# Optimization experiments

Hardware: AMD Instinct MI355X
Metric: run time of the kernel (lower is better)

## Reference

```python
import jax, jax.numpy as jnp
import numpy as np
from jax import lax

MINUS_INF = -1.0e9
BOS, EOS, PAD = 0, 1, 2
NB_LABELS, MAX_DEPTH, EXTRA = 96, 8, 3
STATE = NB_LABELS * MAX_DEPTH + EXTRA  # 771
B, T = 32, 128


def _init_transitions(key):
    t = jax.random.uniform(key, (STATE, STATE), minval=-0.1, maxval=0.1, dtype=jnp.float32)
    # structural constraints from init_weights()
    t = t.at[:, BOS].set(MINUS_INF)          # nothing transitions into BOS
    t = t.at[EOS, :].set(MINUS_INF)          # nothing leaves EOS
    t = t.at[BOS, NB_LABELS + EXTRA:].set(MINUS_INF)  # BOS only into depth-0 states
    t = t.at[NB_LABELS + EXTRA:, EOS].set(MINUS_INF)  # only depth-0 states into EOS
    t = t.at[PAD, :].set(MINUS_INF)
    t = t.at[NB_LABELS + EXTRA:, PAD].set(MINUS_INF)
    t = t.at[PAD, EOS].set(0.0)
    t = t.at[PAD, PAD].set(0.0)
    return t


def setup_inputs() -> dict:
    key = jax.random.key(0)
    k1, k2, k3 = jax.random.split(key, 3)
    emissions = jax.random.normal(k1, (B, T, STATE), dtype=jnp.float32)
    # valid (non-special) states only, so gold-path scores stay finite
    tags = jax.random.randint(k2, (B, T), EXTRA, STATE, dtype=jnp.int64)
    mask = jnp.ones((B, T), dtype=jnp.float32)
    transitions = _init_transitions(k3)
    return {"emissions": emissions, "tags": tags, "mask": mask, "transitions": transitions}


def _crf_nll(emissions, tags, mask, transitions):
    b, t, s = emissions.shape
    tags = tags.astype(jnp.int32)
    batch_idx = jnp.arange(b)

    # ---- gold path score ----
    first = tags[:, 0]
    scores = transitions[BOS, first] + emissions[batch_idx, 0, first]
    prev, cur = tags[:, :-1], tags[:, 1:]
    e_sc = jnp.take_along_axis(emissions[:, 1:], cur[..., None], axis=2)[..., 0]  # (B,T-1)
    t_sc = transitions[prev, cur]                                                 # (B,T-1)
    scores = scores + jnp.sum((e_sc + t_sc) * mask[:, 1:], axis=1)
    last_idx = mask.sum(axis=1).astype(jnp.int32) - 1
    last_tags = tags[batch_idx, last_idx]
    scores = scores + transitions[last_tags, EOS]

    # ---- log partition: forward algorithm (logsumexp DP over S x S) ----
    alphas0 = transitions[BOS][None, :] + emissions[:, 0]  # (B,S)

    def step(alphas, inp):
        em, m = inp  # em: (B,S), m: (B,)
        # (B,S_prev,1) + (S_prev,S_cur) + (B,1,S_cur) -> logsumexp over S_prev
        new = jax.scipy.special.logsumexp(
            alphas[:, :, None] + transitions[None, :, :] + em[:, None, :], axis=1)
        alphas = jnp.where(m[:, None] > 0, new, alphas)
        return alphas, None

    alphas, _ = lax.scan(step, alphas0,
                         (jnp.swapaxes(emissions[:, 1:], 0, 1), mask[:, 1:].T))
    log_z = jax.scipy.special.logsumexp(alphas + transitions[:, EOS][None, :], axis=1)

    # nll = -sum(score - logZ)
    return -jnp.sum(scores - log_z)


def reference(emissions, tags, mask, transitions):
    return _crf_nll(emissions, tags, mask, transitions)
```

## Files before the change

kernel.cpp:

```cpp
#include <hip/hip_runtime.h>
#include <math.h>

typedef unsigned long long u64;
typedef unsigned int u32;

static constexpr int S    = 771;
static constexpr int Tn   = 128;
static constexpr int Bn   = 32;
static constexpr int BOSs = 0;
static constexpr int EOSs = 1;

static constexpr int JB    = 7;
static constexpr int ROWS  = 128;
static constexpr int JPAD  = JB * ROWS;
static constexpr int NW    = 4;
static constexpr int KQ    = JPAD / NW;
static constexpr int KW    = KQ / 4;
static constexpr int KK    = KQ / 16;
static constexpr int NDATA = JPAD / 4;
static constexpr int NMAX  = JB * NW;
static constexpr int XSTR  = 256;
static constexpr int EBLK  = NW * KK * 2 * 64 * 16;
static constexpr int ETOT  = JB * EBLK;
static constexpr float CB  = 8.0f;
static constexpr float C0V = 4.5f;

__device__ __forceinline__ float wave_max_bfly(float v) {
    #pragma unroll
    for (int off = 32; off > 0; off >>= 1) v = fmaxf(v, __shfl_xor(v, off));
    return v;
}
__device__ __forceinline__ float wave_sum_f(float v) {
    #pragma unroll
    for (int off = 32; off > 0; off >>= 1) v += __shfl_down(v, off);
    return v;
}

__device__ __forceinline__ u64 ald64(const u64* p) {
    return __hip_atomic_load((u64*)p, __ATOMIC_RELAXED, __HIP_MEMORY_SCOPE_AGENT);
}
__device__ __forceinline__ void ast64(u64* p, u64 v) {
    __hip_atomic_store(p, v, __ATOMIC_RELAXED, __HIP_MEMORY_SCOPE_AGENT);
}
__device__ __forceinline__ u64 pack(unsigned tag, unsigned payload) {
    return ((u64)tag << 32) | (u64)payload;
}

#if __has_builtin(__builtin_amdgcn_sdot4)
__device__ __forceinline__ int dot4i(unsigned a, unsigned b, int c) {
    return __builtin_amdgcn_sdot4((int)a, (int)b, c, false);
}
#else
__device__ __forceinline__ int dot4i(unsigned a, unsigned b, int c) {
    c += (int)(a & 0xff)         * (int)(b & 0xff);
    c += (int)((a >> 8) & 0xff)  * (int)((b >> 8) & 0xff);
    c += (int)((a >> 16) & 0xff) * (int)((b >> 16) & 0xff);
    c += (int)((a >> 24) & 0xff) * (int)((b >> 24) & 0xff);
    return c;
}
#endif

extern "C" __global__ void build_tabs(const float* __restrict__ trans,
                                      unsigned char* __restrict__ eswz,
                                      float* __restrict__ eteos) {
    int idx = blockIdx.x * blockDim.x + threadIdx.x;
    if (idx < JPAD)
        eteos[idx] = (idx < S) ? __expf(trans[idx * S + EOSs]) : 0.f;
    if (idx >= ETOT) return;
    int e = idx & 15;
    int u = idx >> 4;
    int lane = u & 63;  u >>= 6;
    int rr = u & 1;     u >>= 1;
    int kk = u % KK;
    int h  = u / KK;
    int w  = h & 3, jb = h >> 2;
    int i = w * KQ + kk * 16 + e;
    int j = jb * ROWS + rr * 64 + lane;
    float v = 0.f;
    if (i < S && j < S) v = 115.f * __expf(trans[i * S + j]);
    int q8 = (int)(v + 0.5f);
    if (q8 > 127) q8 = 127;
    eswz[idx] = (unsigned char)q8;
}

__device__ __forceinline__ void publishW(u64* Wp, int jb, int w, unsigned tag,
                                         float af, float C, int lane) {
    float xf = fminf(127.f, 127.f * __expf(af - C));
    int xi = (int)(xf + 0.5f);
    int b0 = __shfl(xi, (4 * lane) & 63);
    int b1 = __shfl(xi, (4 * lane + 1) & 63);
    int b2 = __shfl(xi, (4 * lane + 2) & 63);
    int b3 = __shfl(xi, (4 * lane + 3) & 63);
    unsigned payload = (unsigned)b0 | ((unsigned)b1 << 8)
                     | ((unsigned)b2 << 16) | ((unsigned)b3 << 24);
    float mc = wave_max_bfly(af);
    if (lane < 8)  ast64(Wp + 32 * jb + 8 * w + lane, pack(tag, payload));
    if (lane == 8) ast64(Wp + NDATA + 4 * jb + w,     pack(tag, __float_as_uint(mc)));
}

extern "C" __global__ __attribute__((amdgpu_waves_per_eu(1, 1)))
__launch_bounds__(256)
void crf_fwd(const float* __restrict__ em, const float* __restrict__ mask,
             const float* __restrict__ trans, const int* __restrict__ tags,
             const unsigned char* __restrict__ eswz,
             const float* __restrict__ eteos,
             u64* __restrict__ xb, float* __restrict__ out) {
    const int id  = blockIdx.x;
    const int xcd = id & 7, slot = id >> 3;
    const int jb  = slot % 7;
    const int b   = xcd + 8 * (slot / 7);
    const int tid = threadIdx.x, lane = tid & 63, w = tid >> 6;

    __shared__ __align__(16) u32 strip[NW * KW];
    __shared__ int   part[2][NW][ROWS];
    __shared__ float mred[2][NW];
    __shared__ float cshare;
    __shared__ float redv[NW], redm[NW], redl[NW];

    const float KLOG  = __logf(115.f * 127.f);
    const float KL127 = __logf(127.f);

    const int jrow = jb * ROWS + 32 * w + lane;

    float af = -INFINITY, Cuse = C0V;
    if (lane < 32 && jrow < S)
        af = trans[BOSs * S + jrow] + em[((size_t)b * Tn + 0) * S + jrow];
    publishW(xb + ((size_t)0 * Bn + b) * XSTR, jb, w, 0u, af, C0V, lane);

    uint4 e0[KK], e1[KK];
    {
        const uint4* src = (const uint4*)eswz
                         + ((size_t)(jb * NW + w) * KK * 2) * 64 + lane;
        #pragma unroll
        for (int kk = 0; kk < KK; ++kk) {
            e0[kk] = src[(kk * 2 + 0) * 64];
            e1[kk] = src[(kk * 2 + 1) * 64];
        }
    }
    #pragma unroll
    for (int kk = 0; kk < KK; ++kk) {
        asm volatile("" : "+v"(e0[kk].x), "+v"(e0[kk].y), "+v"(e0[kk].z), "+v"(e0[kk].w));
        asm volatile("" : "+v"(e1[kk].x), "+v"(e1[kk].y), "+v"(e1[kk].z), "+v"(e1[kk].w));
    }

    const bool actd = (lane < KW);
    const bool actm = (lane >= KW) && (lane < KW + 7);

    for (int t = 1; t < Tn; ++t) {
        const u64* R  = xb + ((size_t)((t - 1) & 1) * Bn + b) * XSTR;
        u64*       Wp = xb + ((size_t)((t    ) & 1) * Bn + b) * XSTR;

        float emv = 0.f;
        if (lane < 32 && jrow < S) emv = em[((size_t)b * Tn + t) * S + jrow];
        float mval = mask[b * Tn + t];

        const unsigned tg = (unsigned)(t - 1);
        const u64* pd = R + KW * w + lane;
        const u64* pm = R + NDATA + 7 * w + (lane - KW);
        u64 dc = 0, mc = 0;
        bool okd = !actd, okm = !actm;
        if (actd) dc = ald64(pd);
        if (actm) mc = ald64(pm);
        while (true) {
            if (!okd) okd = ((u32)(dc >> 32) == tg);
            if (!okm) okm = ((u32)(mc >> 32) == tg);
            if (!__any((!okd) | (!okm))) break;
            __builtin_amdgcn_s_sleep(1);
            if (!okd) dc = ald64(pd);
            if (!okm) mc = ald64(pm);
        }

        if (actd) strip[w * KW + lane] = (u32)dc;

        float pmv = actm ? __uint_as_float((u32)mc) : -INFINITY;
        float wmax = wave_max_bfly(pmv);
        if (lane == 0) mred[t & 1][w] = wmax;

        int a0 = 0, a1 = 0;
        const uint4* P4 = (const uint4*)(strip + w * KW);
        #pragma unroll
        for (int kk = 0; kk < KK; ++kk) {
            const uint4 pv = P4[kk];
            a0 = dot4i(e0[kk].x, pv.x, a0);
            a0 = dot4i(e0[kk].y, pv.y, a0);
            a0 = dot4i(e0[kk].z, pv.z, a0);
            a0 = dot4i(e0[kk].w, pv.w, a0);
            a1 = dot4i(e1[kk].x, pv.x, a1);
            a1 = dot4i(e1[kk].y, pv.y, a1);
            a1 = dot4i(e1[kk].z, pv.z, a1);
            a1 = dot4i(e1[kk].w, pv.w, a1);
        }
        part[t & 1][w][lane]      = a0;
        part[t & 1][w][64 + lane] = a1;
        __syncthreads();

        const int p_ = t & 1;
        const int Rr = 32 * w + (lane & 31);
        int s4 = part[p_][0][Rr] + part[p_][1][Rr]
               + part[p_][2][Rr] + part[p_][3][Rr];
        float Cnew = fmaxf(fmaxf(mred[p_][0], mred[p_][1]),
                           fmaxf(mred[p_][2], mred[p_][3])) + CB;
        float nv = Cuse - KLOG + __logf((float)s4) + emv;
        if (lane < 32) af = (mval > 0.f) ? nv : af;
        publishW(Wp, jb, w, (unsigned)t, af, Cnew, lane);
        Cuse = Cnew;
    }

    if (w == 0 && lane == 0) cshare = Cuse;

    if (jb == 0) {
        const u64* R = xb + ((size_t)((Tn - 1) & 1) * Bn + b) * XSTR;
        const unsigned tg = (unsigned)(Tn - 1);
        const bool tact = (tid < NDATA);
        u64 qd = 0;
        bool ok = !tact;
        while (true) {
            if (!ok) { qd = ald64(R + tid); ok = ((u32)(qd >> 32) == tg); }
            if (__syncthreads_and(ok)) break;
        }
        float lsum = 0.f;
        if (tact) {
            unsigned pv = (unsigned)qd;
            int base = 4 * tid;
            lsum = (float)(pv & 0xff)         * eteos[base]
                 + (float)((pv >> 8)  & 0xff) * eteos[base + 1]
                 + (float)((pv >> 16) & 0xff) * eteos[base + 2]
                 + (float)((pv >> 24) & 0xff) * eteos[base + 3];
        }
        float mk = 0.f, val = 0.f;
        if (tid < Tn) {
            mk = mask[b * Tn + tid];
            if (tid > 0) {
                int cur  = tags[b * Tn + tid];
                int prev = tags[b * Tn + tid - 1];
                val = (em[((size_t)b * Tn + tid) * S + cur]
                       + trans[prev * S + cur]) * mk;
            }
        }
        lsum = wave_sum_f(lsum);
        float vs = wave_sum_f(val);
        float ms = wave_sum_f(mk);
        if (lane == 0) { redv[w] = vs; redm[w] = ms; }
        if (lane == 1) redl[w] = lsum;
        __syncthreads();
        if (tid == 0) {
            float tot  = redl[0] + redl[1] + redl[2] + redl[3];
            float logz = cshare - KL127 + __logf(tot);
            float msum = redm[0] + redm[1] + redm[2] + redm[3];
            int last   = (int)(msum + 0.5f) - 1;
            int first  = tags[b * Tn];
            int lastt  = tags[b * Tn + last];
            float score = redv[0] + redv[1] + redv[2] + redv[3]
                        + trans[BOSs * S + first]
                        + em[((size_t)b * Tn) * S + first]
                        + trans[lastt * S + EOSs];
            atomicAdd(out, -(score - logz));
        }
    }
}

extern "C" void kernel_launch(void* const* d_in, const int* in_sizes, int n_in,
                              void* d_out, int out_size, void* d_ws, size_t ws_size,
                              hipStream_t stream) {
    const float* em    = (const float*)d_in[0];
    const int*   tags  = (const int*)d_in[1];
    const float* mask  = (const float*)d_in[2];
    const float* trans = (const float*)d_in[3];
    float* out = (float*)d_out;

    char* ws = (char*)d_ws;
    size_t off = 0;
    unsigned char* eswz = (unsigned char*)(ws + off);
    off += (size_t)ETOT;
    off = (off + 255) & ~(size_t)255;
    float* eteos = (float*)(ws + off); off += JPAD * sizeof(float);
    off = (off + 255) & ~(size_t)255;
    u64* xb = (u64*)(ws + off);        off += (size_t)2 * Bn * XSTR * sizeof(u64);

    (void)hipMemsetAsync(out, 0, sizeof(float), stream);

    build_tabs<<<(ETOT + 255) / 256, 256, 0, stream>>>(trans, eswz, eteos);
    crf_fwd<<<dim3(JB * Bn), 256, 0, stream>>>(em, mask, trans, tags, eswz,
                                               eteos, xb, out);
}
```

Measured before the change: 319.2 us.

## Split K reduction across 8 waves and compute published values in linear domain

Each block now runs 512 threads (8 waves). Every pair of waves splits one quarter of the K dimension, so each wave holds half as many quantized transition registers and performs half as many dot4 ops per timestep. The publish path now builds the int8 payload directly from the linear sum times exp(emission) and a precomputed scale, which removes a log/exp pair. The per-column max is taken from the linear values, and the max reduction is done by one wave instead of through shared memory. In exchange the per-step barrier covers twice as many waves and the final partial-sum reduction adds up eight entries instead of four.

Result: slower. 396.2 us (+24.1%).

```diff
diff --git a/kernel.cpp b/kernel.cpp
--- a/kernel.cpp
+++ b/kernel.cpp
@@ -13,14 +13,14 @@
 static constexpr int JB    = 7;
 static constexpr int ROWS  = 128;
 static constexpr int JPAD  = JB * ROWS;
-static constexpr int NW    = 4;
-static constexpr int KQ    = JPAD / NW;
-static constexpr int KW    = KQ / 4;
-static constexpr int KK    = KQ / 16;
+static constexpr int KQ    = 224;
+static constexpr int KH    = 112;
+static constexpr int KWH   = 28;
+static constexpr int KKH   = 7;
 static constexpr int NDATA = JPAD / 4;
-static constexpr int NMAX  = JB * NW;
+static constexpr int NMAX  = JB * 4;
 static constexpr int XSTR  = 256;
-static constexpr int EBLK  = NW * KK * 2 * 64 * 16;
+static constexpr int EBLK  = 4 * 14 * 2 * 64 * 16;
 static constexpr int ETOT  = JB * EBLK;
 static constexpr float CB  = 8.0f;
 static constexpr float C0V = 4.5f;
@@ -71,10 +71,10 @@
     int u = idx >> 4;
     int lane = u & 63;  u >>= 6;
     int rr = u & 1;     u >>= 1;
-    int kk = u % KK;
-    int h  = u / KK;
-    int w  = h & 3, jb = h >> 2;
-    int i = w * KQ + kk * 16 + e;
+    int kk = u % 14;
+    int h  = u / 14;
+    int q  = h & 3, jb = h >> 2;
+    int i = q * KQ + kk * 16 + e;
     int j = jb * ROWS + rr * 64 + lane;
     float v = 0.f;
     if (i < S && j < S) v = 115.f * __expf(trans[i * S + j]);
@@ -83,7 +83,7 @@
     eswz[idx] = (unsigned char)q8;
 }
 
-__device__ __forceinline__ void publishW(u64* Wp, int jb, int w, unsigned tag,
+__device__ __forceinline__ void publishP(u64* Wp, int jb, int p, unsigned tag,
                                          float af, float C, int lane) {
     float xf = fminf(127.f, 127.f * __expf(af - C));
     int xi = (int)(xf + 0.5f);
@@ -94,12 +94,12 @@
     unsigned payload = (unsigned)b0 | ((unsigned)b1 << 8)
                      | ((unsigned)b2 << 16) | ((unsigned)b3 << 24);
     float mc = wave_max_bfly(af);
-    if (lane < 8)  ast64(Wp + 32 * jb + 8 * w + lane, pack(tag, payload));
-    if (lane == 8) ast64(Wp + NDATA + 4 * jb + w,     pack(tag, __float_as_uint(mc)));
-}
-
-extern "C" __global__ __attribute__((amdgpu_waves_per_eu(1, 1)))
-__launch_bounds__(256)
+    if (lane < 8)  ast64(Wp + 32 * jb + 8 * p + lane, pack(tag, payload));
+    if (lane == 8) ast64(Wp + NDATA + 4 * jb + p,     pack(tag, __float_as_uint(mc)));
+}
+
+extern "C" __global__ __attribute__((amdgpu_waves_per_eu(2, 2)))
+__launch_bounds__(512)
 void crf_fwd(const float* __restrict__ em, const float* __restrict__ mask,
              const float* __restrict__ trans, const int* __restrict__ tags,
              const unsigned char* __restrict__ eswz,
@@ -110,53 +110,55 @@
     const int jb  = slot % 7;
     const int b   = xcd + 8 * (slot / 7);
     const int tid = threadIdx.x, lane = tid & 63, w = tid >> 6;
-
-    __shared__ __align__(16) u32 strip[NW * KW];
-    __shared__ int   part[2][NW][ROWS];
-    __shared__ float mred[2][NW];
+    const int p   = w >> 1, h = w & 1;
+
+    __shared__ __align__(16) u32 strip[8][KWH];
+    __shared__ int   part[2][8][ROWS];
     __shared__ float cshare;
-    __shared__ float redv[NW], redm[NW], redl[NW];
+    __shared__ float redv[8], redm[8], redl[8];
 
     const float KLOG  = __logf(115.f * 127.f);
     const float KL127 = __logf(127.f);
 
-    const int jrow = jb * ROWS + 32 * w + lane;
+    const int jrow = jb * ROWS + 32 * p + lane;
+    const bool erow = (h == 0) && (lane < 32) && (jrow < S);
 
     float af = -INFINITY, Cuse = C0V;
-    if (lane < 32 && jrow < S)
-        af = trans[BOSs * S + jrow] + em[((size_t)b * Tn + 0) * S + jrow];
-    publishW(xb + ((size_t)0 * Bn + b) * XSTR, jb, w, 0u, af, C0V, lane);
-
-    uint4 e0[KK], e1[KK];
+    if (erow) af = trans[BOSs * S + jrow] + em[((size_t)b * Tn + 0) * S + jrow];
+    if (h == 0)
+        publishP(xb + ((size_t)0 * Bn + b) * XSTR, jb, p, 0u, af, C0V, lane);
+
+    uint4 e0[KKH], e1[KKH];
     {
-        const uint4* src = (const uint4*)eswz
-                         + ((size_t)(jb * NW + w) * KK * 2) * 64 + lane;
+        const uint4* base = (const uint4*)eswz + (size_t)(jb * 4 + p) * (14 * 2 * 64);
         #pragma unroll
-        for (int kk = 0; kk < KK; ++kk) {
-            e0[kk] = src[(kk * 2 + 0) * 64];
-            e1[kk] = src[(kk * 2 + 1) * 64];
+        for (int kk = 0; kk < KKH; ++kk) {
+            e0[kk] = base[((7 * h + kk) * 2 + 0) * 64 + lane];
+            e1[kk] = base[((7 * h + kk) * 2 + 1) * 64 + lane];
         }
     }
     #pragma unroll
-    for (int kk = 0; kk < KK; ++kk) {
+    for (int kk = 0; kk < KKH; ++kk) {
         asm volatile("" : "+v"(e0[kk].x), "+v"(e0[kk].y), "+v"(e0[kk].z), "+v"(e0[kk].w));
         asm volatile("" : "+v"(e1[kk].x), "+v"(e1[kk].y), "+v"(e1[kk].z), "+v"(e1[kk].w));
     }
 
-    const bool actd = (lane < KW);
-    const bool actm = (lane >= KW) && (lane < KW + 7);
+    const bool actd = (lane < KWH);
+    const bool actm = (h == 0) && (lane >= KWH) && (lane < KWH + NMAX);
 
     for (int t = 1; t < Tn; ++t) {
         const u64* R  = xb + ((size_t)((t - 1) & 1) * Bn + b) * XSTR;
         u64*       Wp = xb + ((size_t)((t    ) & 1) * Bn + b) * XSTR;
 
-        float emv = 0.f;
-        if (lane < 32 && jrow < S) emv = em[((size_t)b * Tn + t) * S + jrow];
-        float mval = mask[b * Tn + t];
+        float emv = 0.f, pe = 0.f, mval = 0.f;
+        if (h == 0) {
+            if (erow) { emv = em[((size_t)b * Tn + t) * S + jrow]; pe = __expf(emv); }
+            mval = mask[b * Tn + t];
+        }
 
         const unsigned tg = (unsigned)(t - 1);
-        const u64* pd = R + KW * w + lane;
-        const u64* pm = R + NDATA + 7 * w + (lane - KW);
+        const u64* pd = R + KWH * (2 * p + h) + lane;
+        const u64* pm = R + NDATA + (lane - KWH);
         u64 dc = 0, mc = 0;
         bool okd = !actd, okm = !actm;
         if (actd) dc = ald64(pd);
@@ -170,16 +172,19 @@
             if (!okm) mc = ald64(pm);
         }
 
-        if (actd) strip[w * KW + lane] = (u32)dc;
-
-        float pmv = actm ? __uint_as_float((u32)mc) : -INFINITY;
-        float wmax = wave_max_bfly(pmv);
-        if (lane == 0) mred[t & 1][w] = wmax;
+        if (actd) strip[w][lane] = (u32)dc;
+
+        float Cnew = 0.f, kscale = 0.f;
+        if (h == 0) {
+            float mv = actm ? __uint_as_float((u32)mc) : -INFINITY;
+            Cnew = wave_max_bfly(mv) + CB;
+            kscale = __expf(Cuse - Cnew) * (1.0f / 115.0f);
+        }
 
         int a0 = 0, a1 = 0;
-        const uint4* P4 = (const uint4*)(strip + w * KW);
+        const uint4* P4 = (const uint4*)(&strip[w][0]);
         #pragma unroll
-        for (int kk = 0; kk < KK; ++kk) {
+        for (int kk = 0; kk < KKH; ++kk) {
             const uint4 pv = P4[kk];
             a0 = dot4i(e0[kk].x, pv.x, a0);
             a0 = dot4i(e0[kk].y, pv.y, a0);
@@ -194,16 +199,35 @@
         part[t & 1][w][64 + lane] = a1;
         __syncthreads();
 
-        const int p_ = t & 1;
-        const int Rr = 32 * w + (lane & 31);
-        int s4 = part[p_][0][Rr] + part[p_][1][Rr]
-               + part[p_][2][Rr] + part[p_][3][Rr];
-        float Cnew = fmaxf(fmaxf(mred[p_][0], mred[p_][1]),
-                           fmaxf(mred[p_][2], mred[p_][3])) + CB;
-        float nv = Cuse - KLOG + __logf((float)s4) + emv;
-        if (lane < 32) af = (mval > 0.f) ? nv : af;
-        publishW(Wp, jb, w, (unsigned)t, af, Cnew, lane);
-        Cuse = Cnew;
+        if (h == 0) {
+            const int p_ = t & 1;
+            const int Rr = 32 * p + (lane & 31);
+            int s4 = ((part[p_][0][Rr] + part[p_][1][Rr])
+                    + (part[p_][2][Rr] + part[p_][3][Rr]))
+                   + ((part[p_][4][Rr] + part[p_][5][Rr])
+                    + (part[p_][6][Rr] + part[p_][7][Rr]));
+            float xf, mcv;
+            if (mval > 0.f) {
+                float y = (float)s4 * pe;
+                xf = fminf(127.f, y * kscale);
+                float ym = wave_max_bfly(y);
+                mcv = Cuse - KLOG + __logf(ym);
+            } else {
+                xf = fminf(127.f, 127.f * __expf(af - Cnew));
+                mcv = wave_max_bfly(af);
+            }
+            int xi = (int)(xf + 0.5f);
+            int b0 = __shfl(xi, (4 * lane) & 63);
+            int b1 = __shfl(xi, (4 * lane + 1) & 63);
+            int b2 = __shfl(xi, (4 * lane + 2) & 63);
+            int b3 = __shfl(xi, (4 * lane + 3) & 63);
+            unsigned payload = (unsigned)b0 | ((unsigned)b1 << 8)
+                             | ((unsigned)b2 << 16) | ((unsigned)b3 << 24);
+            if (lane < 8)  ast64(Wp + 32 * jb + 8 * p + lane, pack((unsigned)t, payload));
+            if (lane == 8) ast64(Wp + NDATA + 4 * jb + p, pack((unsigned)t, __float_as_uint(mcv)));
+            if (lane < 32) af = (mval > 0.f) ? (Cuse - KLOG + __logf((float)s4) + emv) : af;
+            Cuse = Cnew;
+        }
     }
 
     if (w == 0 && lane == 0) cshare = Cuse;
@@ -244,13 +268,16 @@
         if (lane == 1) redl[w] = lsum;
         __syncthreads();
         if (tid == 0) {
-            float tot  = redl[0] + redl[1] + redl[2] + redl[3];
+            float tot = 0.f, msum = 0.f, vsum = 0.f;
+            #pragma unroll
+            for (int k2 = 0; k2 < 8; ++k2) {
+                tot += redl[k2]; msum += redm[k2]; vsum += redv[k2];
+            }
             float logz = cshare - KL127 + __logf(tot);
-            float msum = redm[0] + redm[1] + redm[2] + redm[3];
             int last   = (int)(msum + 0.5f) - 1;
             int first  = tags[b * Tn];
             int lastt  = tags[b * Tn + last];
-            float score = redv[0] + redv[1] + redv[2] + redv[3]
+            float score = vsum
                         + trans[BOSs * S + first]
                         + em[((size_t)b * Tn) * S + first]
                         + trans[lastt * S + EOSs];
@@ -280,6 +307,6 @@
     (void)hipMemsetAsync(out, 0, sizeof(float), stream);
 
     build_tabs<<<(ETOT + 255) / 256, 256, 0, stream>>>(trans, eswz, eteos);
-    crf_fwd<<<dim3(JB * Bn), 256, 0, stream>>>(em, mask, trans, tags, eswz,
+    crf_fwd<<<dim3(JB * Bn), 512, 0, stream>>>(em, mask, trans, tags, eswz,
                                                eteos, xb, out);
 }
```
